# Kernel optimization log

Hardware: AMD Instinct MI355X
Metric: run time of the kernel (lower is better)

## Reference

```python
import jax, jax.numpy as jnp
import numpy as np

N = 32768; NS = 16; C_MAIN = 128; C_MOD = 128; C_IN = 16; SHARE = 8
EPS = 1e-5; CHUNK = 1024
C_OUT = C_MAIN + C_MOD  # out_main = in_main + in_mod
C_W = C_IN // SHARE     # attention-weight channels = 2


def _bn(x, g, b, m, v):
    # BatchNorm1d in eval mode, per last-dim channel
    return (x - m) / jnp.sqrt(v + EPS) * g + b


def _knn(p, k):
    # exact kNN (self included, distance 0), chunked to bound memory
    def f(q):  # q: (CHUNK, 3)
        d = jnp.sum((q[:, None, :] - p[None, :, :]) ** 2, axis=-1)  # (CHUNK, N)
        return jax.lax.top_k(-d, k)[1]
    return jax.lax.map(f, p.reshape(-1, CHUNK, 3)).reshape(-1, k)


def setup_inputs() -> dict:
    key = jax.random.key(0)
    ks = iter(jax.random.split(key, 24))
    rn = lambda shape, s=0.1: jax.random.normal(next(ks), shape, jnp.float32) * s
    inp = {}
    inp["x_main"] = jax.random.normal(next(ks), (N, C_MAIN), jnp.float32)
    inp["x_mod"] = jax.random.normal(next(ks), (N, C_MOD), jnp.float32)
    inp["xyz"] = jax.random.uniform(next(ks), (N, 3), dtype=jnp.float32)
    inp["W_ein"] = rn((C_OUT, C_IN)); inp["b_ein"] = rn((C_IN,))
    inp["W_eout"] = rn((C_IN, C_OUT)); inp["b_eout"] = rn((C_OUT,))
    inp["Wq"] = rn((C_IN, C_IN)); inp["bq"] = rn((C_IN,))
    inp["Wk"] = rn((C_IN, C_IN)); inp["bk"] = rn((C_IN,))
    inp["Wv"] = rn((C_IN, C_IN)); inp["bv"] = rn((C_IN,))
    inp["Wp1"] = rn((3, 3)); inp["bp1"] = rn((3,))
    inp["Wp2"] = rn((3, C_IN)); inp["bp2"] = rn((C_IN,))
    inp["Wl1"] = rn((C_IN, C_W)); inp["bl1"] = rn((C_W,))
    inp["Wl2"] = rn((C_W, C_W)); inp["bl2"] = rn((C_W,))
    for name, c in (("bn_p", 3), ("bn_w1", C_IN), ("bn_w2", C_W)):
        inp[name + "_g"] = jnp.ones(c, jnp.float32)
        inp[name + "_b"] = jnp.zeros(c, jnp.float32)
        inp[name + "_m"] = jnp.zeros(c, jnp.float32)
        inp[name + "_v"] = jnp.ones(c, jnp.float32)
    return inp


def _forward(x_main, x_mod, xyz, W_ein, b_ein, W_eout, b_eout, Wq, bq, Wk, bk, Wv, bv,
             Wp1, bp1, Wp2, bp2, Wl1, bl1, Wl2, bl2,
             bn_p_g, bn_p_b, bn_p_m, bn_p_v,
             bn_w1_g, bn_w1_b, bn_w1_m, bn_w1_v,
             bn_w2_g, bn_w2_b, bn_w2_m, bn_w2_v, idx):
    x_fused = jnp.concatenate([x_main, x_mod], axis=-1)   # (N, 256)
    x_res = x_fused
    h = x_fused @ W_ein + b_ein                           # E_in: (N, 16)
    # PointTransformerLayer (local vector self-attention over NS neighbors)
    xq = h @ Wq + bq
    xk = h @ Wk + bk
    xv = h @ Wv + bv
    p_r = xyz[idx] - xyz[:, None, :]                      # relative coords (N, NS, 3)
    g_k = xk[idx]                                         # grouped keys   (N, NS, 16)
    g_v = xv[idx]                                         # grouped values (N, NS, 16)
    # linear_p: Linear(3,3) -> BN -> ReLU -> Linear(3, C_IN)
    t = jax.nn.relu(_bn(p_r @ Wp1 + bp1, bn_p_g, bn_p_b, bn_p_m, bn_p_v))
    p_e = t @ Wp2 + bp2                                   # (N, NS, 16)
    # out_planes//mid_planes == 1, so the .view(...).sum(2) on p_e is identity
    w = g_k - xq[:, None, :] + p_e
    # linear_w: BN -> ReLU -> Linear(16,2) -> BN -> ReLU -> Linear(2,2)
    w = jax.nn.relu(_bn(w, bn_w1_g, bn_w1_b, bn_w1_m, bn_w1_v))
    w = w @ Wl1 + bl1
    w = jax.nn.relu(_bn(w, bn_w2_g, bn_w2_b, bn_w2_m, bn_w2_v))
    w = w @ Wl2 + bl2                                     # (N, NS, 2)
    w = jax.nn.softmax(w, axis=1)                         # softmax over neighbors
    agg = ((g_v + p_e).reshape(N, NS, SHARE, C_W) * w[:, :, None, :]).sum(1).reshape(N, C_IN)
    return agg @ W_eout + b_eout + x_res                  # E_out + residual


def reference(x_main, x_mod, xyz, W_ein, b_ein, W_eout, b_eout, Wq, bq, Wk, bk, Wv, bv,
              Wp1, bp1, Wp2, bp2, Wl1, bl1, Wl2, bl2,
              bn_p_g, bn_p_b, bn_p_m, bn_p_v,
              bn_w1_g, bn_w1_b, bn_w1_m, bn_w1_v,
              bn_w2_g, bn_w2_b, bn_w2_m, bn_w2_v):
    idx = _knn(xyz, NS)
    return _forward(x_main, x_mod, xyz, W_ein, b_ein, W_eout, b_eout, Wq, bq, Wk, bk, Wv, bv,
                    Wp1, bp1, Wp2, bp2, Wl1, bl1, Wl2, bl2,
                    bn_p_g, bn_p_b, bn_p_m, bn_p_v,
                    bn_w1_g, bn_w1_b, bn_w1_m, bn_w1_v,
                    bn_w2_g, bn_w2_b, bn_w2_m, bn_w2_v, idx)
```

## Files before the change

### kernel.cpp

```cpp
#include <hip/hip_runtime.h>
#include <cstdint>

#define NPTS 32768
#define K 16
#define G 16
#define NCELL (G*G*G)

typedef unsigned short u16;
typedef unsigned int u32;
typedef unsigned long long u64;

__device__ __forceinline__ float bf(u16 v) { return __uint_as_float(((u32)v) << 16); }
__device__ __forceinline__ void unp(u32 u, float& a, float& b) {
    a = __uint_as_float(u << 16);
    b = __uint_as_float(u & 0xffff0000u);
}
__device__ __forceinline__ u32 f2b(float f) {
    u32 x = __float_as_uint(f);
    return (x + 0x7fffu + ((x >> 16) & 1u)) >> 16;
}
__device__ __forceinline__ u32 pk2(float a, float b) { return f2b(a) | (f2b(b) << 16); }
__device__ __forceinline__ float ldw(const void* p, int j, bool isb) {
    return isb ? bf(((const u16*)p)[j]) : ((const float*)p)[j];
}
__device__ __forceinline__ void ld8(const void* p, size_t i, int cb, bool isb, float xs[8]) {
    if (isb) {
        const uint4* r = (const uint4*)((const u16*)p + i * 128);
        const uint4 u = r[cb];
        unp(u.x, xs[0], xs[1]); unp(u.y, xs[2], xs[3]);
        unp(u.z, xs[4], xs[5]); unp(u.w, xs[6], xs[7]);
    } else {
        const float4* r = (const float4*)((const float*)p + i * 128);
        const float4 a = r[2 * cb], b = r[2 * cb + 1];
        xs[0] = a.x; xs[1] = a.y; xs[2] = a.z; xs[3] = a.w;
        xs[4] = b.x; xs[5] = b.y; xs[6] = b.z; xs[7] = b.w;
    }
}
__device__ __forceinline__ int cellco(float x) {
    int c = (int)(x * (float)G);
    return c < 0 ? 0 : (c > G - 1 ? G - 1 : c);
}
__device__ __forceinline__ u64 shflx64(u64 v, int m) {
    return (u64)__shfl_xor((long long)v, m, 64);
}
__device__ __forceinline__ float dist_np(float4 q, float4 c) {
    const float dx = __fsub_rn(q.x, c.x);
    const float dy = __fsub_rn(q.y, c.y);
    const float dz = __fsub_rn(q.z, c.z);
    return __fadd_rn(__fadd_rn(__fmul_rn(dx, dx), __fmul_rn(dy, dy)), __fmul_rn(dz, dz));
}
__device__ __forceinline__ u64 key64(float d, int idx) {
    return ((u64)__float_as_uint(d) << 32) | (u32)idx;
}

__global__ __launch_bounds__(256) void k_feats(
    const void* __restrict__ xm, const void* __restrict__ xd, const void* __restrict__ xyz,
    const void* __restrict__ Wein, const void* __restrict__ bein,
    const void* __restrict__ Wq, const void* __restrict__ bq,
    const void* __restrict__ Wk, const void* __restrict__ bk,
    const void* __restrict__ Wv, const void* __restrict__ bv,
    const u32* __restrict__ sigp,
    float* __restrict__ oq, u32* __restrict__ okb, u32* __restrict__ ovb,
    float4* __restrict__ xyzf, int* __restrict__ cellCnt,
    int* __restrict__ ptCell, int* __restrict__ ptRank)
{
    const bool isb = (*sigp == 0x3F803F80u);
    __shared__ float sW[4096];
    __shared__ float sM[768];
    __shared__ float sB[64];
    const int t = threadIdx.x;
    for (int u = t; u < 4096; u += 256) sW[u] = ldw(Wein, u, isb);
    if (t < 256) { sM[t] = ldw(Wq, t, isb); sM[256 + t] = ldw(Wk, t, isb); sM[512 + t] = ldw(Wv, t, isb); }
    if (t < 64) {
        const void* bsrc = (t < 16) ? bein : (t < 32) ? bq : (t < 48) ? bk : bv;
        sB[t] = ldw(bsrc, t & 15, isb);
    }
    __syncthreads();
    const int r = blockIdx.x * 128 + (t >> 1);
    const int half = t & 1;
    float hp[16];
#pragma unroll
    for (int j = 0; j < 16; ++j) hp[j] = half ? 0.f : sB[j];
    const void* src = half ? xd : xm;
    const int wbase = half * 128;
#pragma unroll 2
    for (int cb = 0; cb < 16; ++cb) {
        float xs[8];
        ld8(src, (size_t)r, cb, isb, xs);
#pragma unroll
        for (int u = 0; u < 8; ++u) {
            const float x = xs[u];
            const float* w = &sW[(wbase + cb * 8 + u) * 16];
#pragma unroll
            for (int j = 0; j < 16; ++j) hp[j] = fmaf(x, w[j], hp[j]);
        }
    }
    float h[16];
#pragma unroll
    for (int j = 0; j < 16; ++j) h[j] = hp[j] + __shfl_xor(hp[j], 1, 64);
    const float* wm = half ? &sM[256] : &sM[0];
    const float* bm = half ? &sB[32] : &sB[16];
    float acc[16];
#pragma unroll
    for (int j = 0; j < 16; ++j) acc[j] = bm[j];
#pragma unroll
    for (int m = 0; m < 16; ++m) {
        const float hm = h[m];
#pragma unroll
        for (int j = 0; j < 16; ++j) acc[j] = fmaf(hm, wm[m * 16 + j], acc[j]);
    }
    if (half == 0) {
        float4* o4 = (float4*)(oq + (size_t)r * 16);
#pragma unroll
        for (int j4 = 0; j4 < 4; ++j4)
            o4[j4] = make_float4(acc[4 * j4], acc[4 * j4 + 1], acc[4 * j4 + 2], acc[4 * j4 + 3]);
    } else {
        uint4* kr = (uint4*)(okb + (size_t)r * 8);
        kr[0] = make_uint4(pk2(acc[0], acc[1]), pk2(acc[2], acc[3]), pk2(acc[4], acc[5]), pk2(acc[6], acc[7]));
        kr[1] = make_uint4(pk2(acc[8], acc[9]), pk2(acc[10], acc[11]), pk2(acc[12], acc[13]), pk2(acc[14], acc[15]));
    }
    float vacc[8];
    const int vo = half * 8;
#pragma unroll
    for (int u = 0; u < 8; ++u) vacc[u] = sB[48 + vo + u];
#pragma unroll
    for (int m = 0; m < 16; ++m) {
        const float hm = h[m];
#pragma unroll
        for (int u = 0; u < 8; ++u) vacc[u] = fmaf(hm, sM[512 + m * 16 + vo + u], vacc[u]);
    }
    uint4* vr = (uint4*)(ovb + (size_t)r * 8 + half * 4);
    *vr = make_uint4(pk2(vacc[0], vacc[1]), pk2(vacc[2], vacc[3]), pk2(vacc[4], vacc[5]), pk2(vacc[6], vacc[7]));
    if (half == 0) {
        float px, py, pz;
        if (isb) { const u16* z = (const u16*)xyz; px = bf(z[r * 3]); py = bf(z[r * 3 + 1]); pz = bf(z[r * 3 + 2]); }
        else { const float* z = (const float*)xyz; px = z[r * 3]; py = z[r * 3 + 1]; pz = z[r * 3 + 2]; }
        xyzf[r] = make_float4(px, py, pz, 0.f);
        const int c = (cellco(pz) * G + cellco(py)) * G + cellco(px);
        ptCell[r] = c;
        ptRank[r] = atomicAdd(&cellCnt[c], 1);
    }
}

__global__ __launch_bounds__(256) void k_scatter(const float4* __restrict__ xyzf,
    const int* __restrict__ ptCell, const int* __restrict__ ptRank,
    const int* __restrict__ cellCnt, int* __restrict__ starts, float4* __restrict__ sorted)
{
    __shared__ int sSt[NCELL];
    __shared__ int wsum[4];
    const int t = threadIdx.x;
    int c[16];
    {
        const int4* cc = (const int4*)cellCnt;
#pragma unroll
        for (int u = 0; u < 4; ++u) {
            const int4 v = cc[t * 4 + u];
            c[4 * u] = v.x; c[4 * u + 1] = v.y; c[4 * u + 2] = v.z; c[4 * u + 3] = v.w;
        }
    }
    int s = 0;
#pragma unroll
    for (int u = 0; u < 16; ++u) s += c[u];
    int inc = s;
#pragma unroll
    for (int off = 1; off < 64; off <<= 1) {
        const int v = __shfl_up(inc, off, 64);
        if ((t & 63) >= off) inc += v;
    }
    if ((t & 63) == 63) wsum[t >> 6] = inc;
    __syncthreads();
    int pre = 0;
    for (int w = 0; w < (t >> 6); ++w) pre += wsum[w];
    int run = pre + inc - s;
#pragma unroll
    for (int u = 0; u < 16; ++u) { sSt[t * 16 + u] = run; run += c[u]; }
    __syncthreads();
    const int i = blockIdx.x * 256 + t;
    float4 p = xyzf[i];
    p.w = __int_as_float(i);
    sorted[sSt[ptCell[i]] + ptRank[i]] = p;
    if (blockIdx.x == 0) {
#pragma unroll
        for (int u = 0; u < 16; ++u) starts[t * 16 + u] = sSt[t * 16 + u];
        if (t == 0) starts[NCELL] = NPTS;
    }
}

__device__ __forceinline__ void ins16(u64 kb, u64 key[K]) {
    if (kb < key[K - 1]) {
#pragma unroll
        for (int j = 0; j < K; ++j) {
            const bool lt = kb < key[j];
            const u64 tk = lt ? key[j] : kb;
            key[j] = lt ? kb : key[j];
            kb = tk;
        }
    }
}
__device__ __forceinline__ void merge16k(u64 k[K], int mask) {
    u64 pk[K];
#pragma unroll
    for (int i = 0; i < K; ++i) pk[i] = shflx64(k[K - 1 - i], mask);
#pragma unroll
    for (int i = 0; i < K; ++i) k[i] = k[i] < pk[i] ? k[i] : pk[i];
#pragma unroll
    for (int ks = 8; ks >= 1; ks >>= 1) {
#pragma unroll
        for (int i = 0; i < K; ++i) {
            if ((i & ks) == 0) {
                const int j = i + ks;
                const u64 a = k[i], b = k[j];
                k[i] = a < b ? a : b;
                k[j] = a < b ? b : a;
            }
        }
    }
}
__device__ __forceinline__ float guard_radius(float qx, float qy, float qz,
                                              int cx, int cy, int cz, int R)
{
    const float h = 1.0f / (float)G;
    float rg = 3.4e38f;
    if (cx - R >= 1)     rg = fminf(rg, qx - (float)(cx - R) * h);
    if (cx + R <= G - 2) rg = fminf(rg, (float)(cx + R + 1) * h - qx);
    if (cy - R >= 1)     rg = fminf(rg, qy - (float)(cy - R) * h);
    if (cy + R <= G - 2) rg = fminf(rg, (float)(cy + R + 1) * h - qy);
    if (cz - R >= 1)     rg = fminf(rg, qz - (float)(cz - R) * h);
    if (cz + R <= G - 2) rg = fminf(rg, (float)(cz + R + 1) * h - qz);
    return rg;
}
__device__ __forceinline__ void scan_run8(const float4* __restrict__ sorted,
    int b, int e, int l, float4 me, u64 tk, u64 key[K])
{
    int p = b + l;
    if (p >= e) return;
    float4 c = sorted[p];
    while (true) {
        const int pn = p + 8;
        const bool more = pn < e;
        float4 cnx = c;
        if (more) cnx = sorted[pn];
        const u64 kb = key64(dist_np(me, c), __float_as_int(c.w));
        if (kb <= tk) ins16(kb, key);
        if (!more) break;
        c = cnx; p = pn;
    }
}

__global__ __launch_bounds__(256) void k_knng(const float4* __restrict__ sorted,
    const int* __restrict__ starts, int* __restrict__ idxOut)
{
    const int g = blockIdx.x * 256 + threadIdx.x;
    const int s = g >> 3;
    const int l = g & 7;
    const float4 me = sorted[s];
    const int cx = cellco(me.x), cy = cellco(me.y), cz = cellco(me.z);
    const float h = 1.0f / (float)G;

    int rb[9]; int rc[10]; rc[0] = 0;
    {
        const int x0 = cx - 1 < 0 ? 0 : cx - 1;
        const int x1 = cx + 1 > G - 1 ? G - 1 : cx + 1;
#pragma unroll
        for (int r = 0; r < 9; ++r) {
            const int dz = r / 3 - 1, dy = r % 3 - 1;
            const int zz = cz + dz, yy = cy + dy;
            int b = 0, len = 0;
            if ((unsigned)zz <= (unsigned)(G - 1) && (unsigned)yy <= (unsigned)(G - 1)) {
                const int base = (zz * G + yy) * G;
                b = starts[base + x0];
                len = starts[base + x1 + 1] - b;
            }
            rb[r] = b;
            rc[r + 1] = rc[r] + len;
        }
    }
    const int tot = rc[9];
    int bias[9];
#pragma unroll
    for (int r = 0; r < 9; ++r) bias[r] = rb[r] - rc[r];

#define FLAT(f) ({ int _b = bias[0]; \
    _Pragma("unroll") for (int _r = 1; _r < 9; ++_r) _b = ((f) >= rc[_r]) ? bias[_r] : _b; \
    (f) + _b; })

    u64 kA0 = ~0ull, kA1 = ~0ull;
    {
        int p0 = l, p1 = l + 8, p2 = l + 16, p3 = l + 24;
        float4 c0 = sorted[p0 < tot ? FLAT(p0) : 0];
        float4 c1 = sorted[p1 < tot ? FLAT(p1) : 0];
        float4 c2 = sorted[p2 < tot ? FLAT(p2) : 0];
        float4 c3 = sorted[p3 < tot ? FLAT(p3) : 0];
        while (p0 < tot) {
            const int q0 = p0 + 32, q1 = p1 + 32, q2 = p2 + 32, q3 = p3 + 32;
            float4 n0 = sorted[q0 < tot ? FLAT(q0) : 0];
            float4 n1 = sorted[q1 < tot ? FLAT(q1) : 0];
            float4 n2 = sorted[q2 < tot ? FLAT(q2) : 0];
            float4 n3 = sorted[q3 < tot ? FLAT(q3) : 0];
            u64 kb;
#define TOP2(c, valid) \
            kb = (valid) ? key64(dist_np(me, c), __float_as_int((c).w)) : ~0ull; \
            { const bool c0lt = kb < kA0, c1lt = kb < kA1; \
              const u64 nk1 = c0lt ? kA0 : kb; \
              kA1 = c1lt ? nk1 : kA1; \
              kA0 = c0lt ? kb : kA0; }
            TOP2(c0, true);
            TOP2(c1, p1 < tot);
            TOP2(c2, p2 < tot);
            TOP2(c3, p3 < tot);
#undef TOP2
            p0 = q0; p1 = q1; p2 = q2; p3 = q3;
            c0 = n0; c1 = n1; c2 = n2; c3 = n3;
        }
    }
    u64 tau0 = kA1;
#pragma unroll
    for (int m = 1; m <= 4; m <<= 1) { const u64 o = shflx64(tau0, m); tau0 = o > tau0 ? o : tau0; }

    u64 key[K];
#pragma unroll
    for (int j = 0; j < K; ++j) key[j] = ~0ull;
    {
        int p0 = l, p1 = l + 8, p2 = l + 16, p3 = l + 24;
        float4 c0 = sorted[p0 < tot ? FLAT(p0) : 0];
        float4 c1 = sorted[p1 < tot ? FLAT(p1) : 0];
        float4 c2 = sorted[p2 < tot ? FLAT(p2) : 0];
        float4 c3 = sorted[p3 < tot ? FLAT(p3) : 0];
        while (p0 < tot) {
            const int q0 = p0 + 32, q1 = p1 + 32, q2 = p2 + 32, q3 = p3 + 32;
            float4 n0 = sorted[q0 < tot ? FLAT(q0) : 0];
            float4 n1 = sorted[q1 < tot ? FLAT(q1) : 0];
            float4 n2 = sorted[q2 < tot ? FLAT(q2) : 0];
            float4 n3 = sorted[q3 < tot ? FLAT(q3) : 0];
            u64 kb;
#define INSF(c, valid) \
            kb = key64(dist_np(me, c), __float_as_int((c).w)); \
            if ((valid) && kb <= tau0) ins16(kb, key);
            INSF(c0, true);
            INSF(c1, p1 < tot);
            INSF(c2, p2 < tot);
            INSF(c3, p3 < tot);
#undef INSF
            p0 = q0; p1 = q1; p2 = q2; p3 = q3;
            c0 = n0; c1 = n1; c2 = n2; c3 = n3;
        }
    }
#undef FLAT

    merge16k(key, 1); merge16k(key, 2); merge16k(key, 4);

    int R = 1;
    while (R < G) {
        const u64 tk = key[K - 1];
        const float rg = guard_radius(me.x, me.y, me.z, cx, cy, cz, R);
        if (tk < ((u64)__float_as_uint(rg * rg * 0.9999f) << 32)) break;
        if (l != 0) {
#pragma unroll
            for (int j = 0; j < K; ++j) key[j] = ~0ull;
        }
        ++R;
        for (int dz = -R; dz <= R; ++dz) {
            const int zz = cz + dz;
            if ((unsigned)zz > (unsigned)(G - 1)) continue;
            const int az = dz < 0 ? -dz : dz;
            const float dzd = dz < 0 ? me.z - (float)(cz + dz + 1) * h : dz > 0 ? (float)(cz + dz) * h - me.z : 0.f;
            for (int dy = -R; dy <= R; ++dy) {
                const int yy = cy + dy;
                if ((unsigned)yy > (unsigned)(G - 1)) continue;
                const int ay = dy < 0 ? -dy : dy;
                const float dyd = dy < 0 ? me.y - (float)(cy + dy + 1) * h : dy > 0 ? (float)(cy + dy) * h - me.y : 0.f;
                const float myz = dzd * dzd + dyd * dyd;
                const int base = (zz * G + yy) * G;
                if (az == R || ay == R) {
                    if (tk < ((u64)__float_as_uint(myz * 0.9999f) << 32)) continue;
                    const int x0 = cx - R < 0 ? 0 : cx - R;
                    const int x1 = cx + R > G - 1 ? G - 1 : cx + R;
                    scan_run8(sorted, starts[base + x0], starts[base + x1 + 1], l, me, tk, key);
                } else {
                    if (cx - R >= 0) {
                        const float xd = me.x - (float)(cx - R + 1) * h;
                        if (!(tk < ((u64)__float_as_uint((myz + xd * xd) * 0.9999f) << 32)))
                            scan_run8(sorted, starts[base + cx - R], starts[base + cx - R + 1], l, me, tk, key);
                    }
                    if (cx + R <= G - 1) {
                        const float xd = (float)(cx + R) * h - me.x;
                        if (!(tk < ((u64)__float_as_uint((myz + xd * xd) * 0.9999f) << 32)))
                            scan_run8(sorted, starts[base + cx + R], starts[base + cx + R + 1], l, me, tk, key);
                    }
                }
            }
        }
        merge16k(key, 1); merge16k(key, 2); merge16k(key, 4);
    }
    if (l == 0) {
        const int orig = __float_as_int(me.w);
        int4* o = (int4*)(idxOut + (size_t)orig * K);
#pragma unroll
        for (int j4 = 0; j4 < 4; ++j4)
            o[j4] = make_int4((int)(u32)key[4 * j4], (int)(u32)key[4 * j4 + 1],
                              (int)(u32)key[4 * j4 + 2], (int)(u32)key[4 * j4 + 3]);
    }
}

__global__ __launch_bounds__(256) void k_attn(
    const void* __restrict__ xm, const void* __restrict__ xd,
    const float4* __restrict__ xyzf,
    const float* __restrict__ xq, const u32* __restrict__ kbp, const u32* __restrict__ vbp,
    const int* __restrict__ idx,
    const void* __restrict__ Weout, const void* __restrict__ beout,
    const void* __restrict__ Wp1, const void* __restrict__ bp1,
    const void* __restrict__ Wp2, const void* __restrict__ bp2,
    const void* __restrict__ Wl1, const void* __restrict__ bl1,
    const void* __restrict__ Wl2, const void* __restrict__ bl2,
    const void* __restrict__ bnp_g, const void* __restrict__ bnp_b, const void* __restrict__ bnp_m, const void* __restrict__ bnp_v,
    const void* __restrict__ bw1_g, const void* __restrict__ bw1_b, const void* __restrict__ bw1_m, const void* __restrict__ bw1_v,
    const void* __restrict__ bw2_g, const void* __restrict__ bw2_b, const void* __restrict__ bw2_m, const void* __restrict__ bw2_v,
    void* __restrict__ out)
{
    const bool isb = (*(const u32*)bnp_g == 0x3F803F80u);
    __shared__ float sWe[4096];
    __shared__ float sbe[256];
    __shared__ float sWp2[48];
    __shared__ float sbp2[16];
    __shared__ float sWl1[32];
    __shared__ float s1[16], o1[16];
    const int t = threadIdx.x;
    for (int u = t; u < 4096; u += 256) sWe[u] = ldw(Weout, u, isb);
    if (t < 256) sbe[t] = ldw(beout, t, isb);
    if (t < 48) sWp2[t] = ldw(Wp2, t, isb);
    if (t < 16) sbp2[t] = ldw(bp2, t, isb);
    if (t < 32) sWl1[t] = ldw(Wl1, t, isb);
    if (t < 16) {
        const float s = ldw(bw1_g, t, isb) / sqrtf(ldw(bw1_v, t, isb) + 1e-5f);
        s1[t] = s; o1[t] = ldw(bw1_b, t, isb) - ldw(bw1_m, t, isb) * s;
    }
    __syncthreads();
    const int g = blockIdx.x * 256 + t;
    const int s = g >> 3;
    const int l = g & 7;

    const int2 nb2 = ((const int2*)(idx + (size_t)s * 16))[l];
    const uint4* kr0 = (const uint4*)(kbp + (size_t)nb2.x * 8);
    const uint4* kr1 = (const uint4*)(kbp + (size_t)nb2.y * 8);
    const uint4 k0a = kr0[0], k0b = kr0[1];
    const uint4 k1a = kr1[0], k1b = kr1[1];
    const uint4* vr0 = (const uint4*)(vbp + (size_t)nb2.x * 8);
    const uint4* vr1 = (const uint4*)(vbp + (size_t)nb2.y * 8);
    const uint4 v0a = vr0[0], v0b = vr0[1];
    const uint4 v1a = vr1[0], v1b = vr1[1];
    const float4 pp0 = xyzf[nb2.x], pp1 = xyzf[nb2.y];
    const float4 cp = xyzf[s];
    float q[16];
    {
        const float4* qrow = (const float4*)(xq + (size_t)s * 16);
#pragma unroll
        for (int j4 = 0; j4 < 4; ++j4) {
            const float4 v = qrow[j4];
            q[4 * j4] = v.x; q[4 * j4 + 1] = v.y; q[4 * j4 + 2] = v.z; q[4 * j4 + 3] = v.w;
        }
    }
    float xsr[32];
#pragma unroll
    for (int obi = 0; obi < 4; ++obi) {
        const int ob = obi * 8 + l;
        ld8((ob < 16) ? xm : xd, (size_t)s, ob & 15, isb, &xsr[obi * 8]);
    }

    float Wp1r[9], bp1r[3], sp[3], op[3];
#pragma unroll
    for (int u = 0; u < 9; ++u) Wp1r[u] = ldw(Wp1, u, isb);
#pragma unroll
    for (int a = 0; a < 3; ++a) {
        const float sc = ldw(bnp_g, a, isb) / sqrtf(ldw(bnp_v, a, isb) + 1e-5f);
        sp[a] = sc; op[a] = ldw(bnp_b, a, isb) - ldw(bnp_m, a, isb) * sc;
        bp1r[a] = ldw(bp1, a, isb);
    }
    float Wl2r[4], bl1r[2], bl2r[2], s2[2], o2[2];
#pragma unroll
    for (int u = 0; u < 4; ++u) Wl2r[u] = ldw(Wl2, u, isb);
#pragma unroll
    for (int c = 0; c < 2; ++c) {
        bl1r[c] = ldw(bl1, c, isb); bl2r[c] = ldw(bl2, c, isb);
        const float sc = ldw(bw2_g, c, isb) / sqrtf(ldw(bw2_v, c, isb) + 1e-5f);
        s2[c] = sc; o2[c] = ldw(bw2_b, c, isb) - ldw(bw2_m, c, isb) * sc;
    }

    float wa[2], wb[2], ttx[2], tty[2], ttz[2];
#pragma unroll
    for (int n = 0; n < 2; ++n) {
        const float4 pp = n ? pp1 : pp0;
        const float prx = pp.x - cp.x, pry = pp.y - cp.y, prz = pp.z - cp.z;
        float tt[3];
#pragma unroll
        for (int a = 0; a < 3; ++a) {
            float v = prx * Wp1r[a] + pry * Wp1r[3 + a] + prz * Wp1r[6 + a] + bp1r[a];
            v = fmaf(v, sp[a], op[a]);
            tt[a] = v > 0.f ? v : 0.f;
        }
        ttx[n] = tt[0]; tty[n] = tt[1]; ttz[n] = tt[2];
        const uint4 ka = n ? k1a : k0a, kb4 = n ? k1b : k0b;
        float kk[16];
        unp(ka.x, kk[0], kk[1]); unp(ka.y, kk[2], kk[3]); unp(ka.z, kk[4], kk[5]); unp(ka.w, kk[6], kk[7]);
        unp(kb4.x, kk[8], kk[9]); unp(kb4.y, kk[10], kk[11]); unp(kb4.z, kk[12], kk[13]); unp(kb4.w, kk[14], kk[15]);
        float wl0 = bl1r[0], wl1v = bl1r[1];
#pragma unroll
        for (int j = 0; j < 16; ++j) {
            const float pe = tt[0] * sWp2[j] + tt[1] * sWp2[16 + j] + tt[2] * sWp2[32 + j] + sbp2[j];
            float w = kk[j] - q[j] + pe;
            w = fmaf(w, s1[j], o1[j]); w = w > 0.f ? w : 0.f;
            wl0 = fmaf(w, sWl1[2 * j], wl0);
            wl1v = fmaf(w, sWl1[2 * j + 1], wl1v);
        }
        float y0 = fmaf(wl0, s2[0], o2[0]); y0 = y0 > 0.f ? y0 : 0.f;
        float y1 = fmaf(wl1v, s2[1], o2[1]); y1 = y1 > 0.f ? y1 : 0.f;
        wa[n] = y0 * Wl2r[0] + y1 * Wl2r[2] + bl2r[0];
        wb[n] = y0 * Wl2r[1] + y1 * Wl2r[3] + bl2r[1];
    }
    float m0 = fmaxf(wa[0], wa[1]), m1 = fmaxf(wb[0], wb[1]);
#pragma unroll
    for (int m = 1; m <= 4; m <<= 1) {
        m0 = fmaxf(m0, __shfl_xor(m0, m, 64));
        m1 = fmaxf(m1, __shfl_xor(m1, m, 64));
    }
    float sA = 0.f, sB = 0.f;
#pragma unroll
    for (int n = 0; n < 2; ++n) {
        wa[n] = __expf(wa[n] - m0); sA += wa[n];
        wb[n] = __expf(wb[n] - m1); sB += wb[n];
    }
#pragma unroll
    for (int m = 1; m <= 4; m <<= 1) {
        sA += __shfl_xor(sA, m, 64);
        sB += __shfl_xor(sB, m, 64);
    }
    const float rA = 1.f / sA, rB = 1.f / sB;
    float agg[16];
#pragma unroll
    for (int j = 0; j < 16; ++j) agg[j] = 0.f;
#pragma unroll
    for (int n = 0; n < 2; ++n) {
        const float wA = wa[n] * rA, wB = wb[n] * rB;
        const uint4 va = n ? v1a : v0a, vb4 = n ? v1b : v0b;
        float vv[16];
        unp(va.x, vv[0], vv[1]); unp(va.y, vv[2], vv[3]); unp(va.z, vv[4], vv[5]); unp(va.w, vv[6], vv[7]);
        unp(vb4.x, vv[8], vv[9]); unp(vb4.y, vv[10], vv[11]); unp(vb4.z, vv[12], vv[13]); unp(vb4.w, vv[14], vv[15]);
#pragma unroll
        for (int j = 0; j < 16; ++j) {
            const float pe = ttx[n] * sWp2[j] + tty[n] * sWp2[16 + j] + ttz[n] * sWp2[32 + j] + sbp2[j];
            agg[j] = fmaf(vv[j] + pe, (j & 1) ? wB : wA, agg[j]);
        }
    }
#pragma unroll
    for (int j = 0; j < 16; ++j) {
        agg[j] += __shfl_xor(agg[j], 1, 64);
        agg[j] += __shfl_xor(agg[j], 2, 64);
        agg[j] += __shfl_xor(agg[j], 4, 64);
    }
#pragma unroll
    for (int obi = 0; obi < 4; ++obi) {
        const int ob = obi * 8 + l;
        const int o0 = ob * 8;
        float acc[8];
#pragma unroll
        for (int u = 0; u < 8; ++u) acc[u] = sbe[o0 + u] + xsr[obi * 8 + u];
#pragma unroll
        for (int j = 0; j < 16; ++j) {
            const float aj = agg[j];
            const float* w = &sWe[j * 256 + o0];
#pragma unroll
            for (int u = 0; u < 8; ++u) acc[u] = fmaf(aj, w[u], acc[u]);
        }
        if (isb) {
            u32* orow = (u32*)out + (size_t)s * 128;
#pragma unroll
            for (int u = 0; u < 4; ++u)
                orow[ob * 4 + u] = pk2(acc[2 * u], acc[2 * u + 1]);
        } else {
            float4* orow = (float4*)((float*)out + (size_t)s * 256);
            orow[2 * ob]     = make_float4(acc[0], acc[1], acc[2], acc[3]);
            orow[2 * ob + 1] = make_float4(acc[4], acc[5], acc[6], acc[7]);
        }
    }
}

extern "C" void kernel_launch(void* const* d_in, const int* in_sizes, int n_in,
                              void* d_out, int out_size, void* d_ws, size_t ws_size,
                              hipStream_t stream)
{
    (void)in_sizes; (void)n_in; (void)out_size; (void)ws_size;
    const void* xm   = d_in[0];
    const void* xd   = d_in[1];
    const void* xyz  = d_in[2];
    const void* Wein = d_in[3];
    const void* bein = d_in[4];
    const void* Weout= d_in[5];
    const void* beout= d_in[6];
    const void* Wq   = d_in[7];
    const void* bq   = d_in[8];
    const void* Wk   = d_in[9];
    const void* bk   = d_in[10];
    const void* Wv   = d_in[11];
    const void* bv   = d_in[12];
    const void* Wp1  = d_in[13];
    const void* bp1  = d_in[14];
    const void* Wp2  = d_in[15];
    const void* bp2  = d_in[16];
    const void* Wl1  = d_in[17];
    const void* bl1  = d_in[18];
    const void* Wl2  = d_in[19];
    const void* bl2  = d_in[20];
    const void* bnp_g = d_in[21];
    const void* bnp_b = d_in[22];
    const void* bnp_m = d_in[23];
    const void* bnp_v = d_in[24];
    const void* bw1_g = d_in[25];
    const void* bw1_b = d_in[26];
    const void* bw1_m = d_in[27];
    const void* bw1_v = d_in[28];
    const void* bw2_g = d_in[29];
    const void* bw2_b = d_in[30];
    const void* bw2_m = d_in[31];
    const void* bw2_v = d_in[32];

    char* ws = (char*)d_ws;
    const size_t MB = 1024 * 1024;
    float*  oq    = (float*)(ws);
    u32*    okb   = (u32*) (ws + 2 * MB);
    u32*    ovb   = (u32*) (ws + 3 * MB);
    int*    idx   = (int*) (ws + 4 * MB);
    float4* xyzf  = (float4*)(ws + 6 * MB);
    float4* sortp = (float4*)(ws + 6 * MB + 512 * 1024);
    int* cellCnt  = (int*)(ws + 7 * MB);
    int* starts   = (int*)(ws + 7 * MB + 32 * 1024);
    int* ptCell   = (int*)(ws + 7 * MB + 64 * 1024);
    int* ptRank   = (int*)(ws + 7 * MB + 192 * 1024);

    hipMemsetAsync(cellCnt, 0, NCELL * sizeof(int), stream);
    k_feats<<<dim3(NPTS * 2 / 256), dim3(256), 0, stream>>>(
        xm, xd, xyz, Wein, bein, Wq, bq, Wk, bk, Wv, bv,
        (const u32*)bnp_g, oq, okb, ovb, xyzf, cellCnt, ptCell, ptRank);
    k_scatter<<<dim3(NPTS / 256), dim3(256), 0, stream>>>(xyzf, ptCell, ptRank, cellCnt, starts, sortp);
    k_knng<<<dim3(NPTS * 8 / 256), dim3(256), 0, stream>>>(sortp, starts, idx);
    k_attn<<<dim3(NPTS * 8 / 256), dim3(256), 0, stream>>>(
        xm, xd, xyzf, oq, okb, ovb, idx, Weout, beout, Wp1, bp1, Wp2, bp2,
        Wl1, bl1, Wl2, bl2, bnp_g, bnp_b, bnp_m, bnp_v,
        bw1_g, bw1_b, bw1_m, bw1_v, bw2_g, bw2_b, bw2_m, bw2_v, d_out);
}
```

Before: 259.2 us.

## Permute per-point features into spatial-cell order and swizzle blocks across XCDs

The scatter kernel now also copies q, k and v rows into cell-sorted order and records an original-to-sorted index map. kNN writes neighbour indices in sorted space, and the attention kernel runs per sorted point, so neighbour k/v/xyz gathers hit nearby memory. Residual inputs are read and outputs written through the original index. Both kNN and attention remap block IDs so that each XCD works on a contiguous range of sorted points, which should improve L2 locality. The cost is an extra permutation copy of roughly 4 MB, plus scattered residual and output accesses.

```diff
diff --git a/kernel.cpp b/kernel.cpp
--- a/kernel.cpp
+++ b/kernel.cpp
@@ -144,7 +144,10 @@
 
 __global__ __launch_bounds__(256) void k_scatter(const float4* __restrict__ xyzf,
     const int* __restrict__ ptCell, const int* __restrict__ ptRank,
-    const int* __restrict__ cellCnt, int* __restrict__ starts, float4* __restrict__ sorted)
+    const int* __restrict__ cellCnt, int* __restrict__ starts, float4* __restrict__ sorted,
+    const float* __restrict__ oq, const u32* __restrict__ okb, const u32* __restrict__ ovb,
+    float* __restrict__ qs, u32* __restrict__ ks, u32* __restrict__ vs,
+    int* __restrict__ o2s)
 {
     __shared__ int sSt[NCELL];
     __shared__ int wsum[4];
@@ -176,9 +179,22 @@
     for (int u = 0; u < 16; ++u) { sSt[t * 16 + u] = run; run += c[u]; }
     __syncthreads();
     const int i = blockIdx.x * 256 + t;
+    const int dst = sSt[ptCell[i]] + ptRank[i];
     float4 p = xyzf[i];
     p.w = __int_as_float(i);
-    sorted[sSt[ptCell[i]] + ptRank[i]] = p;
+    sorted[dst] = p;
+    o2s[i] = dst;
+    {
+        const float4* q4 = (const float4*)(oq + (size_t)i * 16);
+        float4* qd = (float4*)(qs + (size_t)dst * 16);
+        qd[0] = q4[0]; qd[1] = q4[1]; qd[2] = q4[2]; qd[3] = q4[3];
+        const uint4* kr = (const uint4*)(okb + (size_t)i * 8);
+        uint4* kd = (uint4*)(ks + (size_t)dst * 8);
+        kd[0] = kr[0]; kd[1] = kr[1];
+        const uint4* vr = (const uint4*)(ovb + (size_t)i * 8);
+        uint4* vd = (uint4*)(vs + (size_t)dst * 8);
+        vd[0] = vr[0]; vd[1] = vr[1];
+    }
     if (blockIdx.x == 0) {
 #pragma unroll
         for (int u = 0; u < 16; ++u) starts[t * 16 + u] = sSt[t * 16 + u];
@@ -248,9 +264,11 @@
 }
 
 __global__ __launch_bounds__(256) void k_knng(const float4* __restrict__ sorted,
-    const int* __restrict__ starts, int* __restrict__ idxOut)
+    const int* __restrict__ starts, const int* __restrict__ o2s, int* __restrict__ idxS)
 {
-    const int g = blockIdx.x * 256 + threadIdx.x;
+    const int b = blockIdx.x;
+    const int bs = (b & 7) * ((int)gridDim.x >> 3) + (b >> 3);
+    const int g = bs * 256 + threadIdx.x;
     const int s = g >> 3;
     const int l = g & 7;
     const float4 me = sorted[s];
@@ -265,13 +283,13 @@
         for (int r = 0; r < 9; ++r) {
             const int dz = r / 3 - 1, dy = r % 3 - 1;
             const int zz = cz + dz, yy = cy + dy;
-            int b = 0, len = 0;
+            int bb = 0, len = 0;
             if ((unsigned)zz <= (unsigned)(G - 1) && (unsigned)yy <= (unsigned)(G - 1)) {
                 const int base = (zz * G + yy) * G;
-                b = starts[base + x0];
-                len = starts[base + x1 + 1] - b;
+                bb = starts[base + x0];
+                len = starts[base + x1 + 1] - bb;
             }
-            rb[r] = b;
+            rb[r] = bb;
             rc[r + 1] = rc[r] + len;
         }
     }
@@ -393,20 +411,20 @@
         merge16k(key, 1); merge16k(key, 2); merge16k(key, 4);
     }
     if (l == 0) {
-        const int orig = __float_as_int(me.w);
-        int4* o = (int4*)(idxOut + (size_t)orig * K);
-#pragma unroll
-        for (int j4 = 0; j4 < 4; ++j4)
-            o[j4] = make_int4((int)(u32)key[4 * j4], (int)(u32)key[4 * j4 + 1],
-                              (int)(u32)key[4 * j4 + 2], (int)(u32)key[4 * j4 + 3]);
+        int4* o = (int4*)(idxS + (size_t)s * K);
+#pragma unroll
+        for (int j4 = 0; j4 < 4; ++j4) {
+            o[j4] = make_int4(o2s[(u32)key[4 * j4]], o2s[(u32)key[4 * j4 + 1]],
+                              o2s[(u32)key[4 * j4 + 2]], o2s[(u32)key[4 * j4 + 3]]);
+        }
     }
 }
 
 __global__ __launch_bounds__(256) void k_attn(
     const void* __restrict__ xm, const void* __restrict__ xd,
-    const float4* __restrict__ xyzf,
-    const float* __restrict__ xq, const u32* __restrict__ kbp, const u32* __restrict__ vbp,
-    const int* __restrict__ idx,
+    const float4* __restrict__ sortp,
+    const float* __restrict__ qs, const u32* __restrict__ kbp, const u32* __restrict__ vbp,
+    const int* __restrict__ idxS,
     const void* __restrict__ Weout, const void* __restrict__ beout,
     const void* __restrict__ Wp1, const void* __restrict__ bp1,
     const void* __restrict__ Wp2, const void* __restrict__ bp2,
@@ -435,11 +453,15 @@
         s1[t] = s; o1[t] = ldw(bw1_b, t, isb) - ldw(bw1_m, t, isb) * s;
     }
     __syncthreads();
-    const int g = blockIdx.x * 256 + t;
+    const int b = blockIdx.x;
+    const int bs = (b & 7) * ((int)gridDim.x >> 3) + (b >> 3);
+    const int g = bs * 256 + t;
     const int s = g >> 3;
     const int l = g & 7;
 
-    const int2 nb2 = ((const int2*)(idx + (size_t)s * 16))[l];
+    const float4 cp = sortp[s];
+    const int orig = __float_as_int(cp.w);
+    const int2 nb2 = ((const int2*)(idxS + (size_t)s * 16))[l];
     const uint4* kr0 = (const uint4*)(kbp + (size_t)nb2.x * 8);
     const uint4* kr1 = (const uint4*)(kbp + (size_t)nb2.y * 8);
     const uint4 k0a = kr0[0], k0b = kr0[1];
@@ -448,11 +470,10 @@
     const uint4* vr1 = (const uint4*)(vbp + (size_t)nb2.y * 8);
     const uint4 v0a = vr0[0], v0b = vr0[1];
     const uint4 v1a = vr1[0], v1b = vr1[1];
-    const float4 pp0 = xyzf[nb2.x], pp1 = xyzf[nb2.y];
-    const float4 cp = xyzf[s];
+    const float4 pp0 = sortp[nb2.x], pp1 = sortp[nb2.y];
     float q[16];
     {
-        const float4* qrow = (const float4*)(xq + (size_t)s * 16);
+        const float4* qrow = (const float4*)(qs + (size_t)s * 16);
 #pragma unroll
         for (int j4 = 0; j4 < 4; ++j4) {
             const float4 v = qrow[j4];
@@ -463,7 +484,7 @@
 #pragma unroll
     for (int obi = 0; obi < 4; ++obi) {
         const int ob = obi * 8 + l;
-        ld8((ob < 16) ? xm : xd, (size_t)s, ob & 15, isb, &xsr[obi * 8]);
+        ld8((ob < 16) ? xm : xd, (size_t)orig, ob & 15, isb, &xsr[obi * 8]);
     }
 
     float Wp1r[9], bp1r[3], sp[3], op[3];
@@ -571,12 +592,11 @@
             for (int u = 0; u < 8; ++u) acc[u] = fmaf(aj, w[u], acc[u]);
         }
         if (isb) {
-            u32* orow = (u32*)out + (size_t)s * 128;
-#pragma unroll
-            for (int u = 0; u < 4; ++u)
-                orow[ob * 4 + u] = pk2(acc[2 * u], acc[2 * u + 1]);
+            uint4* orow = (uint4*)((u32*)out + (size_t)orig * 128);
+            orow[ob] = make_uint4(pk2(acc[0], acc[1]), pk2(acc[2], acc[3]),
+                                  pk2(acc[4], acc[5]), pk2(acc[6], acc[7]));
         } else {
-            float4* orow = (float4*)((float*)out + (size_t)s * 256);
+            float4* orow = (float4*)((float*)out + (size_t)orig * 256);
             orow[2 * ob]     = make_float4(acc[0], acc[1], acc[2], acc[3]);
             orow[2 * ob + 1] = make_float4(acc[4], acc[5], acc[6], acc[7]);
         }
@@ -627,22 +647,27 @@
     float*  oq    = (float*)(ws);
     u32*    okb   = (u32*) (ws + 2 * MB);
     u32*    ovb   = (u32*) (ws + 3 * MB);
-    int*    idx   = (int*) (ws + 4 * MB);
-    float4* xyzf  = (float4*)(ws + 6 * MB);
-    float4* sortp = (float4*)(ws + 6 * MB + 512 * 1024);
-    int* cellCnt  = (int*)(ws + 7 * MB);
-    int* starts   = (int*)(ws + 7 * MB + 32 * 1024);
-    int* ptCell   = (int*)(ws + 7 * MB + 64 * 1024);
-    int* ptRank   = (int*)(ws + 7 * MB + 192 * 1024);
+    int*    idxS  = (int*) (ws + 4 * MB);
+    float*  qs    = (float*)(ws + 6 * MB);
+    u32*    ks    = (u32*) (ws + 8 * MB);
+    u32*    vs    = (u32*) (ws + 9 * MB);
+    float4* xyzf  = (float4*)(ws + 10 * MB);
+    float4* sortp = (float4*)(ws + 10 * MB + 512 * 1024);
+    int* cellCnt  = (int*)(ws + 11 * MB);
+    int* starts   = (int*)(ws + 11 * MB + 32 * 1024);
+    int* ptCell   = (int*)(ws + 11 * MB + 64 * 1024);
+    int* ptRank   = (int*)(ws + 11 * MB + 192 * 1024);
+    int* o2s      = (int*)(ws + 11 * MB + 320 * 1024);
 
     hipMemsetAsync(cellCnt, 0, NCELL * sizeof(int), stream);
     k_feats<<<dim3(NPTS * 2 / 256), dim3(256), 0, stream>>>(
         xm, xd, xyz, Wein, bein, Wq, bq, Wk, bk, Wv, bv,
         (const u32*)bnp_g, oq, okb, ovb, xyzf, cellCnt, ptCell, ptRank);
-    k_scatter<<<dim3(NPTS / 256), dim3(256), 0, stream>>>(xyzf, ptCell, ptRank, cellCnt, starts, sortp);
-    k_knng<<<dim3(NPTS * 8 / 256), dim3(256), 0, stream>>>(sortp, starts, idx);
+    k_scatter<<<dim3(NPTS / 256), dim3(256), 0, stream>>>(
+        xyzf, ptCell, ptRank, cellCnt, starts, sortp, oq, okb, ovb, qs, ks, vs, o2s);
+    k_knng<<<dim3(NPTS * 8 / 256), dim3(256), 0, stream>>>(sortp, starts, o2s, idxS);
     k_attn<<<dim3(NPTS * 8 / 256), dim3(256), 0, stream>>>(
-        xm, xd, xyzf, oq, okb, ovb, idx, Weout, beout, Wp1, bp1, Wp2, bp2,
+        xm, xd, sortp, qs, ks, vs, idxS, Weout, beout, Wp1, bp1, Wp2, bp2,
         Wl1, bl1, Wl2, bl2, bnp_g, bnp_b, bnp_m, bnp_v,
         bw1_g, bw1_b, bw1_m, bw1_v, bw2_g, bw2_b, bw2_m, bw2_v, d_out);
 }
```

Result: no change. 258.0 us (-0.5%).
